# Kernel optimization log

Hardware: AMD Instinct MI355X
Metric: run time of the kernel (lower is better)

## Reference

```python
import jax, jax.numpy as jnp
import numpy as np

B, L, H, N, A = 1024, 50, 256, 100000, 100

def setup_inputs() -> dict:
    key = jax.random.key(0)
    k1, k2, k3, k4, k5, k6 = jax.random.split(key, 6)
    stdv = 1.0 / np.sqrt(H)
    u = lambda k, shp: jax.random.uniform(k, shp, jnp.float32, -stdv, stdv)
    inputs = jax.random.randint(k1, (B, L), 0, N)
    masks = jnp.ones((B, L), jnp.float32)
    return {
        'inputs': inputs,
        'masks': masks,
        'emb': u(k2, (N, H)),
        'Qw': u(k3, (A, H)),
        'Kw': u(k4, (A, H)),
        'lin_w': u(k5, (H, 2 * H)),
        'lin_b': u(k6, (H,)),
    }

def reference(inputs, masks, emb, Qw, Kw, lin_w, lin_b):
    x = emb[inputs]                                   # [B,L,H]
    Q = jax.nn.sigmoid(jnp.einsum('blh,ah->bla', x, Qw))   # [B,L,A]
    K = jax.nn.sigmoid(jnp.einsum('blh,ah->bla', x, Kw))
    affinity = jnp.einsum('bla,bma->blm', Q, K) / jnp.sqrt(jnp.float32(A))  # [B,L,L]
    # remove diagonal (affinity - diag_embed(diagonal))
    eye = jnp.eye(L, dtype=affinity.dtype)
    masked_affinity = affinity * (1.0 - eye)
    col_masked = masked_affinity * masks[:, None, :]  # column mask
    item_score = jnp.sum(col_masked, axis=2) * masks  # [B,L]
    item_score = jax.nn.softmax(item_score, axis=1) * masks
    item_score = item_score / jnp.sum(item_score, axis=1, keepdims=True)
    att_final = jnp.sum(item_score[:, :, None] * x, axis=1)  # [B,H]
    # last valid item per session
    lengths = masks.sum(axis=1).astype(jnp.int32)
    last_id = jnp.take_along_axis(inputs, (lengths - 1)[:, None], axis=1)[:, 0]
    last_emb = emb[last_id]                           # [B,H]
    final_rep = jnp.concatenate([att_final, last_emb], axis=1) @ lin_w.T + lin_b  # [B,H]
    scores = final_rep @ emb[1:].T                    # [B,N-1]
    return scores, affinity
```

## Files before the change

### kernel.cpp

```cpp
#include <hip/hip_runtime.h>
#include <hip/hip_bf16.h>

#define BB 1024
#define LL 50
#define HH 256
#define AA 100
#define NN 100000
#define NM1 99999

typedef short short8 __attribute__((ext_vector_type(8)));
typedef float f32x4 __attribute__((ext_vector_type(4)));

__device__ __forceinline__ float wave_sum(float v) {
#pragma unroll
  for (int off = 32; off; off >>= 1) v += __shfl_xor(v, off, 64);
  return v;
}
__device__ __forceinline__ float wave_max(float v) {
#pragma unroll
  for (int off = 32; off; off >>= 1) v = fmaxf(v, __shfl_xor(v, off, 64));
  return v;
}
__device__ __forceinline__ short f2bf(float f) {
  union { __hip_bfloat16 h; short s; } u;
  u.h = __float2bfloat16(f);
  return u.s;
}

__global__ __launch_bounds__(256) void session_kernel(
    const int* __restrict__ inputs, const float* __restrict__ masks,
    const float* __restrict__ emb, const float* __restrict__ Qw,
    const float* __restrict__ Kw, const float* __restrict__ lin_w,
    const float* __restrict__ lin_b, float* __restrict__ out_aff,
    short* __restrict__ frb) {
  __shared__ float s_x[LL][HH];
  __shared__ __hip_bfloat16 s_q[LL][AA + 4];
  __shared__ __hip_bfloat16 s_kT[AA][LL + 2];
  __shared__ float s_mask[LL];
  __shared__ int s_idx[LL];
  __shared__ float s_row[LL];
  __shared__ float s_p[LL];
  __shared__ float s_cat[2 * HH];
  __shared__ int s_last;

  const int b = blockIdx.x;
  const int tid = threadIdx.x;

  if (tid < LL) {
    s_idx[tid] = inputs[b * LL + tid];
    s_mask[tid] = masks[b * LL + tid];
  }
  __syncthreads();

  for (int u = tid; u < LL * (HH / 4); u += 256) {
    int l = u >> 6, c = u & 63;
    ((float4*)&s_x[l][0])[c] = ((const float4*)(emb + (size_t)s_idx[l] * HH))[c];
  }
  __syncthreads();

  if (tid < 2 * AA) {
    const float* W = (tid < AA) ? (Qw + tid * HH) : (Kw + (tid - AA) * HH);
    float acc[LL];
#pragma unroll
    for (int l = 0; l < LL; ++l) acc[l] = 0.f;
    for (int k0 = 0; k0 < HH; k0 += 8) {
      float4 w0 = *(const float4*)(W + k0);
      float4 w1 = *(const float4*)(W + k0 + 4);
#pragma unroll
      for (int l = 0; l < LL; ++l) {
        float4 x0 = *(const float4*)&s_x[l][k0];
        float4 x1 = *(const float4*)&s_x[l][k0 + 4];
        acc[l] += w0.x * x0.x + w0.y * x0.y + w0.z * x0.z + w0.w * x0.w +
                  w1.x * x1.x + w1.y * x1.y + w1.z * x1.z + w1.w * x1.w;
      }
    }
    if (tid < AA) {
#pragma unroll
      for (int l = 0; l < LL; ++l)
        s_q[l][tid] = __float2bfloat16(1.f / (1.f + expf(-acc[l])));
    } else {
      const int a = tid - AA;
#pragma unroll
      for (int l = 0; l < LL; ++l)
        s_kT[a][l] = __float2bfloat16(1.f / (1.f + expf(-acc[l])));
    }
  }
  __syncthreads();

  {
    const int wv = tid >> 6;
    const int m = tid & 63;
    for (int l = wv; l < LL; l += 4) {
      float acc = 0.f;
      if (m < LL) {
#pragma unroll 10
        for (int a = 0; a < AA; ++a)
          acc += __bfloat162float(s_q[l][a]) * __bfloat162float(s_kT[a][m]);
      }
      const float aff = acc * 0.1f;
      if (m < LL) out_aff[(size_t)b * (LL * LL) + l * LL + m] = aff;
      const float am = (m < LL && m != l) ? aff * s_mask[m] : 0.f;
      const float tot = wave_sum(am);
      if (m == 0) s_row[l] = tot * s_mask[l];
    }
  }
  __syncthreads();

  if (tid < 64) {
    const int l = tid;
    const float mk = (l < LL) ? s_mask[l] : 0.f;
    const float v = (l < LL) ? s_row[l] : -3.4e38f;
    const float mx = wave_max(v);
    const float e = (l < LL) ? expf(v - mx) : 0.f;
    const float s1 = wave_sum(e);
    float p = e / s1 * mk;
    const float s2 = wave_sum(p);
    p /= s2;
    if (l < LL) s_p[l] = p;
    const float cnt = wave_sum(mk);
    if (l == 0) s_last = s_idx[(int)(cnt + 0.5f) - 1];
  }
  __syncthreads();

  {
    const int h = tid;
    float acc = 0.f;
#pragma unroll
    for (int l = 0; l < LL; ++l) acc += s_p[l] * s_x[l][h];
    s_cat[h] = acc;
    s_cat[HH + h] = emb[(size_t)s_last * HH + h];
  }
  __syncthreads();

  {
    const int h = tid;
    float acc = lin_b[h];
    const float4* lw = (const float4*)(lin_w + (size_t)h * (2 * HH));
#pragma unroll 16
    for (int j = 0; j < (2 * HH) / 4; ++j) {
      float4 w = lw[j];
      float4 cv = *(const float4*)&s_cat[j * 4];
      acc += w.x * cv.x + w.y * cv.y + w.z * cv.z + w.w * cv.w;
    }
    frb[(size_t)b * HH + h] = f2bf(acc);
  }
}

#define NBLK 782
__global__ __launch_bounds__(256) void scores_kernel(
    const short* __restrict__ frb, const float* __restrict__ emb,
    float* __restrict__ out) {
  __shared__ short As[128 * 256];
  __shared__ short Bs[128 * 256];

  const int tid = threadIdx.x;
  const int wg = blockIdx.x;
  const int p = (wg & 7) * NBLK + (wg >> 3);
  const int m0 = (p & 7) * 128;
  const int n0 = (p >> 3) * 128;

#pragma unroll
  for (int i = 0; i < 16; ++i) {
    const int idx = tid + i * 256;
    const int r = idx >> 5, c = idx & 31;
    int byte = ((r << 9) | (c << 4)) ^ ((r & 7) << 4);
    *(short8*)((char*)As + byte) =
        *(const short8*)(frb + (((size_t)(m0 + r)) << 8) + (c << 3));
  }
#pragma unroll
  for (int i = 0; i < 16; ++i) {
    const int idx = tid + i * 256;
    const int r = idx >> 5, c = idx & 31;
    int er = 1 + n0 + r;
    if (er > NM1) er = NM1;
    const float* s = emb + (((size_t)er) << 8) + (c << 3);
    const float4 f0 = *(const float4*)s;
    const float4 f1 = *(const float4*)(s + 4);
    short8 v;
    v[0] = f2bf(f0.x); v[1] = f2bf(f0.y); v[2] = f2bf(f0.z); v[3] = f2bf(f0.w);
    v[4] = f2bf(f1.x); v[5] = f2bf(f1.y); v[6] = f2bf(f1.z); v[7] = f2bf(f1.w);
    int byte = ((r << 9) | (c << 4)) ^ ((r & 7) << 4);
    *(short8*)((char*)Bs + byte) = v;
  }
  __syncthreads();

  const int lane = tid & 63;
  const int wv = tid >> 6;
  const int wr = wv >> 1, wc = wv & 1;
  const int l15 = lane & 15, lg = lane >> 4;

  f32x4 acc[4][4];
#pragma unroll
  for (int fm = 0; fm < 4; ++fm)
#pragma unroll
    for (int fn = 0; fn < 4; ++fn) acc[fm][fn] = (f32x4)(0.f);

#pragma unroll
  for (int ks = 0; ks < 8; ++ks) {
    const int kb = ks * 64 + (lg << 4);
    short8 af[4], bf[4];
#pragma unroll
    for (int f = 0; f < 4; ++f) {
      const int Ra = wr * 64 + f * 16 + l15;
      const int ba = ((Ra << 9) + kb) ^ ((Ra & 7) << 4);
      af[f] = *(const short8*)((const char*)As + ba);
      const int Rb = wc * 64 + f * 16 + l15;
      const int bb = ((Rb << 9) + kb) ^ ((Rb & 7) << 4);
      bf[f] = *(const short8*)((const char*)Bs + bb);
    }
#pragma unroll
    for (int fm = 0; fm < 4; ++fm)
#pragma unroll
      for (int fn = 0; fn < 4; ++fn)
        acc[fm][fn] = __builtin_amdgcn_mfma_f32_16x16x32_bf16(
            af[fm], bf[fn], acc[fm][fn], 0, 0, 0);
  }

#pragma unroll
  for (int fm = 0; fm < 4; ++fm) {
    const int mrow = m0 + wr * 64 + fm * 16 + lg * 4;
#pragma unroll
    for (int fn = 0; fn < 4; ++fn) {
      const int n = n0 + wc * 64 + fn * 16 + l15;
      if (n < NM1) {
#pragma unroll
        for (int j = 0; j < 4; ++j)
          out[(size_t)(mrow + j) * NM1 + n] = acc[fm][fn][j];
      }
    }
  }
}

extern "C" void kernel_launch(void* const* d_in, const int* in_sizes, int n_in,
                              void* d_out, int out_size, void* d_ws,
                              size_t ws_size, hipStream_t stream) {
  const int* inputs = (const int*)d_in[0];
  const float* masks = (const float*)d_in[1];
  const float* emb = (const float*)d_in[2];
  const float* Qw = (const float*)d_in[3];
  const float* Kw = (const float*)d_in[4];
  const float* lin_w = (const float*)d_in[5];
  const float* lin_b = (const float*)d_in[6];

  float* out_scores = (float*)d_out;
  float* out_aff = out_scores + (size_t)BB * NM1;
  short* frb = (short*)d_ws;

  session_kernel<<<dim3(BB), dim3(256), 0, stream>>>(
      inputs, masks, emb, Qw, Kw, lin_w, lin_b, out_aff, frb);

  scores_kernel<<<dim3(8 * NBLK), dim3(256), 0, stream>>>(frb, emb, out_scores);
}
```

Baseline: 913.4 us.

## Use MFMA for session projections and affinity; halve scores LDS tiles

The session kernel now stores gathered embeddings as bf16 in swizzled LDS. The Q/K projections and the QK^T affinity run on bf16 MFMA instead of scalar FP32 loops, and row sums are reduced through per-wave partials. The scores kernel splits K=256 into two 128-wide halves, halving LDS per block to 64KB so more blocks can be resident per CU, at the cost of an extra barrier and reload phase. Using bf16 for x and the weights in the projections adds rounding error compared with the previous FP32 path.

```diff
diff --git a/kernel.cpp b/kernel.cpp
--- a/kernel.cpp
+++ b/kernel.cpp
@@ -26,6 +26,11 @@
   u.h = __float2bfloat16(f);
   return u.s;
 }
+__device__ __forceinline__ float bf2f(short s) {
+  union { short s; __hip_bfloat16 h; } u;
+  u.s = s;
+  return __bfloat162float(u.h);
+}
 
 __global__ __launch_bounds__(256) void session_kernel(
     const int* __restrict__ inputs, const float* __restrict__ masks,
@@ -33,83 +38,150 @@
     const float* __restrict__ Kw, const float* __restrict__ lin_w,
     const float* __restrict__ lin_b, float* __restrict__ out_aff,
     short* __restrict__ frb) {
-  __shared__ float s_x[LL][HH];
-  __shared__ __hip_bfloat16 s_q[LL][AA + 4];
-  __shared__ __hip_bfloat16 s_kT[AA][LL + 2];
-  __shared__ float s_mask[LL];
-  __shared__ int s_idx[LL];
-  __shared__ float s_row[LL];
-  __shared__ float s_p[LL];
+  __shared__ short s_xb[64 * 256];
+  __shared__ short s_q[64 * 128];
+  __shared__ short s_k[64 * 128];
+  __shared__ float s_mask[64];
+  __shared__ int s_idx[64];
+  __shared__ float s_rowp[4][64];
+  __shared__ float s_p[64];
   __shared__ float s_cat[2 * HH];
   __shared__ int s_last;
 
   const int b = blockIdx.x;
   const int tid = threadIdx.x;
-
-  if (tid < LL) {
-    s_idx[tid] = inputs[b * LL + tid];
-    s_mask[tid] = masks[b * LL + tid];
-  }
-  __syncthreads();
-
-  for (int u = tid; u < LL * (HH / 4); u += 256) {
-    int l = u >> 6, c = u & 63;
-    ((float4*)&s_x[l][0])[c] = ((const float4*)(emb + (size_t)s_idx[l] * HH))[c];
-  }
-  __syncthreads();
-
-  if (tid < 2 * AA) {
-    const float* W = (tid < AA) ? (Qw + tid * HH) : (Kw + (tid - AA) * HH);
-    float acc[LL];
-#pragma unroll
-    for (int l = 0; l < LL; ++l) acc[l] = 0.f;
-    for (int k0 = 0; k0 < HH; k0 += 8) {
-      float4 w0 = *(const float4*)(W + k0);
-      float4 w1 = *(const float4*)(W + k0 + 4);
-#pragma unroll
-      for (int l = 0; l < LL; ++l) {
-        float4 x0 = *(const float4*)&s_x[l][k0];
-        float4 x1 = *(const float4*)&s_x[l][k0 + 4];
-        acc[l] += w0.x * x0.x + w0.y * x0.y + w0.z * x0.z + w0.w * x0.w +
-                  w1.x * x1.x + w1.y * x1.y + w1.z * x1.z + w1.w * x1.w;
+  const int lane = tid & 63;
+  const int wv = tid >> 6;
+  const int l15 = lane & 15;
+  const int lg = lane >> 4;
+
+  if (tid < 64) s_mask[tid] = (tid < LL) ? masks[b * LL + tid] : 0.f;
+  if (tid < LL) s_idx[tid] = inputs[b * LL + tid];
+#pragma unroll
+  for (int i = 0; i < 4; ++i) {
+    short8 z = {};
+    ((short8*)s_q)[tid + i * 256] = z;
+    ((short8*)s_k)[tid + i * 256] = z;
+  }
+  __syncthreads();
+
+  for (int u = tid; u < LL * 32; u += 256) {
+    const int r = u >> 5, c = u & 31;
+    const float* s = emb + (size_t)s_idx[r] * HH + c * 8;
+    const float4 f0 = *(const float4*)s;
+    const float4 f1 = *(const float4*)(s + 4);
+    short8 v;
+    v[0] = f2bf(f0.x); v[1] = f2bf(f0.y); v[2] = f2bf(f0.z); v[3] = f2bf(f0.w);
+    v[4] = f2bf(f1.x); v[5] = f2bf(f1.y); v[6] = f2bf(f1.z); v[7] = f2bf(f1.w);
+    const int byte = ((r << 9) | (c << 4)) ^ ((r & 7) << 4);
+    *(short8*)((char*)s_xb + byte) = v;
+  }
+  __syncthreads();
+
+  f32x4 acc[4][4];
+#pragma unroll
+  for (int i = 0; i < 4; ++i)
+#pragma unroll
+    for (int j = 0; j < 4; ++j) acc[i][j] = (f32x4)(0.f);
+
+#pragma unroll
+  for (int ks = 0; ks < 8; ++ks) {
+    const int kb = (ks * 32 + lg * 8) * 2;
+    short8 af[4];
+#pragma unroll
+    for (int mf = 0; mf < 4; ++mf) {
+      const int r = mf * 16 + l15;
+      af[mf] = *(const short8*)((const char*)s_xb +
+                                (((r << 9) + kb) ^ ((r & 7) << 4)));
+    }
+#pragma unroll
+    for (int nfi = 0; nfi < 4; ++nfi) {
+      const int nf = wv + 4 * nfi;
+      const float* Wp = (nf < 7) ? Qw : Kw;
+      int arow = (nf < 7) ? nf * 16 + l15 : (nf - 7) * 16 + l15;
+      if (nf >= 14) arow = 0;
+      if (arow > AA - 1) arow = AA - 1;
+      const float* s = Wp + (size_t)arow * HH + ks * 32 + lg * 8;
+      const float4 w0 = *(const float4*)s;
+      const float4 w1 = *(const float4*)(s + 4);
+      short8 bf;
+      bf[0] = f2bf(w0.x); bf[1] = f2bf(w0.y); bf[2] = f2bf(w0.z); bf[3] = f2bf(w0.w);
+      bf[4] = f2bf(w1.x); bf[5] = f2bf(w1.y); bf[6] = f2bf(w1.z); bf[7] = f2bf(w1.w);
+#pragma unroll
+      for (int mf = 0; mf < 4; ++mf)
+        acc[nfi][mf] =
+            __builtin_amdgcn_mfma_f32_16x16x32_bf16(af[mf], bf, acc[nfi][mf], 0, 0, 0);
+    }
+  }
+#pragma unroll
+  for (int nfi = 0; nfi < 4; ++nfi) {
+    const int nf = wv + 4 * nfi;
+#pragma unroll
+    for (int mf = 0; mf < 4; ++mf)
+#pragma unroll
+      for (int j = 0; j < 4; ++j) {
+        const int row = mf * 16 + lg * 4 + j;
+        const float sg = 1.f / (1.f + expf(-acc[nfi][mf][j]));
+        if (row < LL && nf < 14) {
+          if (nf < 7) {
+            const int a = nf * 16 + l15;
+            if (a < AA)
+              *(short*)((char*)s_q + (((row << 8) + a * 2) ^ ((row & 7) << 4))) =
+                  f2bf(sg);
+          } else {
+            const int a = (nf - 7) * 16 + l15;
+            if (a < AA)
+              *(short*)((char*)s_k + (((row << 8) + a * 2) ^ ((row & 7) << 4))) =
+                  f2bf(sg);
+          }
+        }
       }
-    }
-    if (tid < AA) {
-#pragma unroll
-      for (int l = 0; l < LL; ++l)
-        s_q[l][tid] = __float2bfloat16(1.f / (1.f + expf(-acc[l])));
-    } else {
-      const int a = tid - AA;
-#pragma unroll
-      for (int l = 0; l < LL; ++l)
-        s_kT[a][l] = __float2bfloat16(1.f / (1.f + expf(-acc[l])));
-    }
-  }
-  __syncthreads();
-
+  }
+  __syncthreads();
+
+  f32x4 c4[4];
+#pragma unroll
+  for (int i = 0; i < 4; ++i) c4[i] = (f32x4)(0.f);
+#pragma unroll
+  for (int ks = 0; ks < 4; ++ks) {
+    const int kb = (ks * 32 + lg * 8) * 2;
+    const int mrow = wv * 16 + l15;
+    const short8 kf = *(const short8*)((const char*)s_k +
+                                       (((mrow << 8) + kb) ^ ((mrow & 7) << 4)));
+#pragma unroll
+    for (int mf = 0; mf < 4; ++mf) {
+      const int r = mf * 16 + l15;
+      const short8 qf = *(const short8*)((const char*)s_q +
+                                         (((r << 8) + kb) ^ ((r & 7) << 4)));
+      c4[mf] = __builtin_amdgcn_mfma_f32_16x16x32_bf16(qf, kf, c4[mf], 0, 0, 0);
+    }
+  }
   {
-    const int wv = tid >> 6;
-    const int m = tid & 63;
-    for (int l = wv; l < LL; l += 4) {
-      float acc = 0.f;
-      if (m < LL) {
-#pragma unroll 10
-        for (int a = 0; a < AA; ++a)
-          acc += __bfloat162float(s_q[l][a]) * __bfloat162float(s_kT[a][m]);
+    const int col = wv * 16 + l15;
+#pragma unroll
+    for (int mf = 0; mf < 4; ++mf)
+#pragma unroll
+      for (int j = 0; j < 4; ++j) {
+        const int row = mf * 16 + lg * 4 + j;
+        const float val = c4[mf][j] * 0.1f;
+        if (row < LL && col < LL)
+          out_aff[(size_t)b * (LL * LL) + row * LL + col] = val;
+        float am = (col < LL && col != row) ? val * s_mask[col] : 0.f;
+        am += __shfl_xor(am, 1, 64);
+        am += __shfl_xor(am, 2, 64);
+        am += __shfl_xor(am, 4, 64);
+        am += __shfl_xor(am, 8, 64);
+        if (l15 == 0) s_rowp[wv][row] = am;
       }
-      const float aff = acc * 0.1f;
-      if (m < LL) out_aff[(size_t)b * (LL * LL) + l * LL + m] = aff;
-      const float am = (m < LL && m != l) ? aff * s_mask[m] : 0.f;
-      const float tot = wave_sum(am);
-      if (m == 0) s_row[l] = tot * s_mask[l];
-    }
   }
   __syncthreads();
 
   if (tid < 64) {
     const int l = tid;
-    const float mk = (l < LL) ? s_mask[l] : 0.f;
-    const float v = (l < LL) ? s_row[l] : -3.4e38f;
+    const float mk = s_mask[l];
+    float v = -3.4e38f;
+    if (l < LL)
+      v = (s_rowp[0][l] + s_rowp[1][l] + s_rowp[2][l] + s_rowp[3][l]) * mk;
     const float mx = wave_max(v);
     const float e = (l < LL) ? expf(v - mx) : 0.f;
     const float s1 = wave_sum(e);
@@ -124,25 +196,29 @@
 
   {
     const int h = tid;
-    float acc = 0.f;
-#pragma unroll
-    for (int l = 0; l < LL; ++l) acc += s_p[l] * s_x[l][h];
-    s_cat[h] = acc;
+    float a = 0.f;
+#pragma unroll
+    for (int l = 0; l < LL; ++l) {
+      const short xv = *(const short*)((const char*)s_xb +
+                                       ((((l << 9) + h * 2)) ^ ((l & 7) << 4)));
+      a += s_p[l] * bf2f(xv);
+    }
+    s_cat[h] = a;
     s_cat[HH + h] = emb[(size_t)s_last * HH + h];
   }
   __syncthreads();
 
   {
     const int h = tid;
-    float acc = lin_b[h];
+    float acc2 = lin_b[h];
     const float4* lw = (const float4*)(lin_w + (size_t)h * (2 * HH));
 #pragma unroll 16
     for (int j = 0; j < (2 * HH) / 4; ++j) {
-      float4 w = lw[j];
-      float4 cv = *(const float4*)&s_cat[j * 4];
-      acc += w.x * cv.x + w.y * cv.y + w.z * cv.z + w.w * cv.w;
-    }
-    frb[(size_t)b * HH + h] = f2bf(acc);
+      const float4 w = lw[j];
+      const float4 cv = *(const float4*)&s_cat[j * 4];
+      acc2 += w.x * cv.x + w.y * cv.y + w.z * cv.z + w.w * cv.w;
+    }
+    frb[(size_t)b * HH + h] = f2bf(acc2);
   }
 }
 
@@ -150,8 +226,8 @@
 __global__ __launch_bounds__(256) void scores_kernel(
     const short* __restrict__ frb, const float* __restrict__ emb,
     float* __restrict__ out) {
-  __shared__ short As[128 * 256];
-  __shared__ short Bs[128 * 256];
+  __shared__ short As[128 * 128];
+  __shared__ short Bs[128 * 128];
 
   const int tid = threadIdx.x;
   const int wg = blockIdx.x;
@@ -159,31 +235,6 @@
   const int m0 = (p & 7) * 128;
   const int n0 = (p >> 3) * 128;
 
-#pragma unroll
-  for (int i = 0; i < 16; ++i) {
-    const int idx = tid + i * 256;
-    const int r = idx >> 5, c = idx & 31;
-    int byte = ((r << 9) | (c << 4)) ^ ((r & 7) << 4);
-    *(short8*)((char*)As + byte) =
-        *(const short8*)(frb + (((size_t)(m0 + r)) << 8) + (c << 3));
-  }
-#pragma unroll
-  for (int i = 0; i < 16; ++i) {
-    const int idx = tid + i * 256;
-    const int r = idx >> 5, c = idx & 31;
-    int er = 1 + n0 + r;
-    if (er > NM1) er = NM1;
-    const float* s = emb + (((size_t)er) << 8) + (c << 3);
-    const float4 f0 = *(const float4*)s;
-    const float4 f1 = *(const float4*)(s + 4);
-    short8 v;
-    v[0] = f2bf(f0.x); v[1] = f2bf(f0.y); v[2] = f2bf(f0.z); v[3] = f2bf(f0.w);
-    v[4] = f2bf(f1.x); v[5] = f2bf(f1.y); v[6] = f2bf(f1.z); v[7] = f2bf(f1.w);
-    int byte = ((r << 9) | (c << 4)) ^ ((r & 7) << 4);
-    *(short8*)((char*)Bs + byte) = v;
-  }
-  __syncthreads();
-
   const int lane = tid & 63;
   const int wv = tid >> 6;
   const int wr = wv >> 1, wc = wv & 1;
@@ -195,25 +246,46 @@
 #pragma unroll
     for (int fn = 0; fn < 4; ++fn) acc[fm][fn] = (f32x4)(0.f);
 
-#pragma unroll
-  for (int ks = 0; ks < 8; ++ks) {
-    const int kb = ks * 64 + (lg << 4);
-    short8 af[4], bf[4];
-#pragma unroll
-    for (int f = 0; f < 4; ++f) {
-      const int Ra = wr * 64 + f * 16 + l15;
-      const int ba = ((Ra << 9) + kb) ^ ((Ra & 7) << 4);
-      af[f] = *(const short8*)((const char*)As + ba);
-      const int Rb = wc * 64 + f * 16 + l15;
-      const int bb = ((Rb << 9) + kb) ^ ((Rb & 7) << 4);
-      bf[f] = *(const short8*)((const char*)Bs + bb);
-    }
-#pragma unroll
-    for (int fm = 0; fm < 4; ++fm)
-#pragma unroll
-      for (int fn = 0; fn < 4; ++fn)
-        acc[fm][fn] = __builtin_amdgcn_mfma_f32_16x16x32_bf16(
-            af[fm], bf[fn], acc[fm][fn], 0, 0, 0);
+  for (int kh = 0; kh < 2; ++kh) {
+    if (kh) __syncthreads();
+#pragma unroll
+    for (int i = 0; i < 8; ++i) {
+      const int idx = tid + i * 256;
+      const int r = idx >> 4, c = idx & 15;
+      const int byte = ((r << 8) | (c << 4)) ^ ((r & 7) << 4);
+      *(short8*)((char*)As + byte) =
+          *(const short8*)(frb + (((size_t)(m0 + r)) << 8) + kh * 128 + (c << 3));
+      int er = 1 + n0 + r;
+      if (er > NM1) er = NM1;
+      const float* s = emb + (((size_t)er) << 8) + kh * 128 + (c << 3);
+      const float4 f0 = *(const float4*)s;
+      const float4 f1 = *(const float4*)(s + 4);
+      short8 v;
+      v[0] = f2bf(f0.x); v[1] = f2bf(f0.y); v[2] = f2bf(f0.z); v[3] = f2bf(f0.w);
+      v[4] = f2bf(f1.x); v[5] = f2bf(f1.y); v[6] = f2bf(f1.z); v[7] = f2bf(f1.w);
+      *(short8*)((char*)Bs + byte) = v;
+    }
+    __syncthreads();
+#pragma unroll
+    for (int ks = 0; ks < 4; ++ks) {
+      const int kb = ks * 64 + lg * 16;
+      short8 af[4], bf[4];
+#pragma unroll
+      for (int f = 0; f < 4; ++f) {
+        const int Ra = wr * 64 + f * 16 + l15;
+        af[f] = *(const short8*)((const char*)As +
+                                 (((Ra << 8) + kb) ^ ((Ra & 7) << 4)));
+        const int Rb = wc * 64 + f * 16 + l15;
+        bf[f] = *(const short8*)((const char*)Bs +
+                                 (((Rb << 8) + kb) ^ ((Rb & 7) << 4)));
+      }
+#pragma unroll
+      for (int fm = 0; fm < 4; ++fm)
+#pragma unroll
+        for (int fn = 0; fn < 4; ++fn)
+          acc[fm][fn] = __builtin_amdgcn_mfma_f32_16x16x32_bf16(
+              af[fm], bf[fn], acc[fm][fn], 0, 0, 0);
+    }
   }
 
 #pragma unroll
```

Result: faster. 814.1 us (-10.9%).
